# Kernel optimization log

Hardware: AMD Instinct MI355X
Metric: run time of the kernel (lower is better)

## Reference

```python
import jax, jax.numpy as jnp
import numpy as np
import math

B, H, S, D = 2, 16, 4096, 64

def setup_inputs() -> dict:
    key = jax.random.key(0)
    kq, kk, kv = jax.random.split(key, 3)
    q = jax.random.normal(kq, (B, H, S, D), dtype=jnp.float32)
    k = jax.random.normal(kk, (B, H, S, D), dtype=jnp.float32)
    v = jax.random.normal(kv, (B, H, S, D), dtype=jnp.float32)
    # causal mask: True above the diagonal means 'masked out' (matches masked_fill_)
    mask = ~jnp.tril(jnp.ones((S, S), dtype=bool))
    return {"q": q, "k": k, "v": v, "mask": mask}

def reference(q, k, v, mask):
    head_dim = q.shape[-1]
    scale = 1.0 / math.sqrt(head_dim)
    # scores: [B, H, S, S] -- same math as the chunked torch loop (chunking is a no-op mathematically)
    scores = jnp.einsum('bhqd,bhkd->bhqk', q, k) * scale
    scores = jnp.where(mask[None, None, :, :], -jnp.inf, scores)
    attn = jax.nn.softmax(scores, axis=-1)
    return jnp.einsum('bhqk,bhkd->bhqd', attn, v)
```

## Files before the change

kernel.cpp:

```cpp
#include <hip/hip_runtime.h>
#include <hip/hip_bf16.h>
#include <math.h>

#define SLEN 4096
#define DH   64
#define KVB  64
#define NHEAD 32
#define QBLK 128
#define NQT   (SLEN / QBLK)
#define TILE_E (KVB * DH)

typedef float  f32x4 __attribute__((ext_vector_type(4)));
typedef short  bf16x8 __attribute__((ext_vector_type(8)));
typedef unsigned short u16x8 __attribute__((ext_vector_type(8)));
typedef unsigned short u16x4 __attribute__((ext_vector_type(4)));
union U8 { u16x8 u; bf16x8 b; };
union U4 { unsigned d[4]; bf16x8 b; };

__device__ inline unsigned short f2bf(float f) {
    return __builtin_bit_cast(unsigned short, __float2bfloat16(f));
}
__device__ inline unsigned pk2(float lo, float hi_) {
    return (unsigned)f2bf(lo) | ((unsigned)f2bf(hi_) << 16);
}

__device__ inline void gload16(const unsigned short* g, unsigned short* l) {
    __builtin_amdgcn_global_load_lds(
        (const __attribute__((address_space(1))) void*)g,
        (__attribute__((address_space(3))) void*)l, 16, 0, 0);
}

extern "C" __global__ __launch_bounds__(512)
void prep_kv(const float* __restrict__ K, const float* __restrict__ V,
             unsigned short* __restrict__ Kb, unsigned short* __restrict__ Vt)
{
    const int tile = blockIdx.x & 63;
    const int head = blockIdx.x >> 6;
    const size_t gbase = (size_t)head * SLEN * DH + (size_t)tile * KVB * DH;
    const size_t tbase = ((size_t)head * 64 + tile) * TILE_E;
    const int tid = threadIdx.x;
    if (blockIdx.y == 0) {
        const int row = tid >> 3, d0 = (tid & 7) * 8;
        const float* src = K + gbase + (size_t)row * DH + d0;
        f32x4 a = *(const f32x4*)src, b = *(const f32x4*)(src + 4);
        u16x8 o;
        #pragma unroll
        for (int j = 0; j < 4; ++j) { o[j] = f2bf(a[j]); o[4 + j] = f2bf(b[j]); }
        *(u16x8*)&Kb[tbase + row * 64 + ((unsigned)d0 ^ ((row & 7) << 3))] = o;
    } else {
        const int kk = tid & 63, d0 = (tid >> 6) * 8;
        const int pos = ((kk >> 5) << 5) | (((kk & 15) >> 2) << 3)
                      | (((kk >> 4) & 1) << 2) | (kk & 3);
        const float* src = V + gbase + (size_t)kk * DH + d0;
        f32x4 a = *(const f32x4*)src, b = *(const f32x4*)(src + 4);
        #pragma unroll
        for (int j = 0; j < 8; ++j) {
            const int d = d0 + j;
            const float x = (j < 4) ? a[j] : b[j - 4];
            Vt[tbase + d * 64 + ((unsigned)pos ^ ((d & 7) << 3))] = f2bf(x);
        }
    }
}

extern "C" __global__ __launch_bounds__(256, 4)
void fa_fwd_v19(const float* __restrict__ Q, float* __restrict__ O,
                const unsigned short* __restrict__ Kb,
                const unsigned short* __restrict__ Vt)
{
    const int tid  = threadIdx.x;
    const int lane = tid & 63;
    const int w    = tid >> 6;
    const int l15  = lane & 15;
    const int l4   = lane >> 4;

    const int bid  = (int)blockIdx.x;
    const int i32  = bid >> 5;
    const int qt   = (i32 < 16) ? (2 * i32) : (63 - 2 * i32);
    const int head = bid & 31;
    const size_t qbase  = (size_t)head * SLEN * DH;
    const size_t kvbase = (size_t)head * 64 * TILE_E;

    __shared__ __align__(16) unsigned short Kl[3][TILE_E];
    __shared__ __align__(16) unsigned short Vl[2][TILE_E];

    const float QSC = 0.125f * 1.44269504088896340736f;

    U8 ones;
    #pragma unroll
    for (int j = 0; j < 8; ++j) ones.u[j] = 0x3F80;

    const unsigned short* ksrc = Kb + kvbase;
    const unsigned short* vsrc = Vt + kvbase;

    const int q0   = qt * QBLK;
    const int ntl  = 2 * qt + 2;
    const int wg0  = q0 + w * 16;
    const int wg1  = q0 + 64 + w * 16;
    const int qg0  = wg0 + l15;
    const int qg1  = wg1 + l15;

    auto stageK = [&](int b, int t) {
        const size_t toff = (size_t)t * TILE_E;
        const int ib = w * 2;
        gload16(ksrc + toff + ib * 512 + lane * 8,       &Kl[b][ib * 512]);
        gload16(ksrc + toff + (ib + 1) * 512 + lane * 8, &Kl[b][(ib + 1) * 512]);
    };
    auto stageV = [&](int b, int t) {
        const size_t toff = (size_t)t * TILE_E;
        const int ib = w * 2;
        gload16(vsrc + toff + ib * 512 + lane * 8,       &Vl[b][ib * 512]);
        gload16(vsrc + toff + (ib + 1) * 512 + lane * 8, &Vl[b][(ib + 1) * 512]);
    };

    stageK(0, 0);
    stageV(0, 0);
    stageK(1, 1);

    bf16x8 aq0[2], aq1[2];
    {
        const float* qp0 = Q + qbase + (size_t)qg0 * DH + l4 * 8;
        const float* qp1 = Q + qbase + (size_t)qg1 * DH + l4 * 8;
        #pragma unroll
        for (int ch = 0; ch < 2; ++ch) {
            f32x4 f0 = *(const f32x4*)(qp0 + ch * 32);
            f32x4 f1 = *(const f32x4*)(qp0 + ch * 32 + 4);
            U4 u;
            u.d[0] = pk2(f0[0] * QSC, f0[1] * QSC);
            u.d[1] = pk2(f0[2] * QSC, f0[3] * QSC);
            u.d[2] = pk2(f1[0] * QSC, f1[1] * QSC);
            u.d[3] = pk2(f1[2] * QSC, f1[3] * QSC);
            aq0[ch] = u.b;
            f0 = *(const f32x4*)(qp1 + ch * 32);
            f1 = *(const f32x4*)(qp1 + ch * 32 + 4);
            u.d[0] = pk2(f0[0] * QSC, f0[1] * QSC);
            u.d[1] = pk2(f0[2] * QSC, f0[3] * QSC);
            u.d[2] = pk2(f1[0] * QSC, f1[1] * QSC);
            u.d[3] = pk2(f1[2] * QSC, f1[3] * QSC);
            aq1[ch] = u.b;
        }
    }

    f32x4 acc0[4] = {}, acc1[4] = {};
    f32x4 lrow0 = {}, lrow1 = {};

    int kb = 0, vb = 0;
    for (int t = 0; t < ntl; ++t) {
        const int k0 = t * KVB;
        if (t + 1 < ntl) asm volatile("s_waitcnt vmcnt(2)" ::: "memory");
        else             asm volatile("s_waitcnt vmcnt(0)" ::: "memory");
        __builtin_amdgcn_s_barrier();

        if (t + 1 < ntl) stageV(vb ^ 1, t + 1);
        if (t + 2 < ntl) stageK((kb == 0) ? 2 : kb - 1, t + 2);

        {
            const bool live0 = (k0 <= wg0 + 15);
            const unsigned short* Kc = &Kl[kb][0];
            const unsigned short* Vc = &Vl[vb][0];

            __builtin_amdgcn_s_setprio(1);
            f32x4 s0[4], s1[4];
            #pragma unroll
            for (int nt = 0; nt < 4; ++nt) {
                const int row = nt * 16 + l15;
                const unsigned rb = (unsigned)row * 64, sw = (unsigned)((row & 7) << 3);
                U8 ak0, ak1;
                ak0.u = *(const u16x8*)&Kc[rb + ((unsigned)(l4 * 8) ^ sw)];
                ak1.u = *(const u16x8*)&Kc[rb + ((unsigned)(32 + l4 * 8) ^ sw)];
                if (live0) {
                    f32x4 z = {};
                    z = __builtin_amdgcn_mfma_f32_16x16x32_bf16(ak0.b, aq0[0], z, 0, 0, 0);
                    s0[nt] = __builtin_amdgcn_mfma_f32_16x16x32_bf16(ak1.b, aq0[1], z, 0, 0, 0);
                }
                f32x4 z1 = {};
                z1 = __builtin_amdgcn_mfma_f32_16x16x32_bf16(ak0.b, aq1[0], z1, 0, 0, 0);
                s1[nt] = __builtin_amdgcn_mfma_f32_16x16x32_bf16(ak1.b, aq1[1], z1, 0, 0, 0);
            }
            __builtin_amdgcn_s_setprio(0);

            if (live0 && (k0 + KVB - 1 > wg0)) {
                #pragma unroll
                for (int nt = 0; nt < 4; ++nt)
                    #pragma unroll
                    for (int r = 0; r < 4; ++r)
                        if (k0 + nt * 16 + l4 * 4 + r > qg0) s0[nt][r] = -INFINITY;
            }
            if (k0 + KVB - 1 > wg1) {
                #pragma unroll
                for (int nt = 0; nt < 4; ++nt)
                    #pragma unroll
                    for (int r = 0; r < 4; ++r)
                        if (k0 + nt * 16 + l4 * 4 + r > qg1) s1[nt][r] = -INFINITY;
            }

            U4 u00, u01, u10, u11;
            if (live0) {
                u00.d[0] = pk2(exp2f(s0[0][0]), exp2f(s0[0][1]));
                u00.d[1] = pk2(exp2f(s0[0][2]), exp2f(s0[0][3]));
                u00.d[2] = pk2(exp2f(s0[1][0]), exp2f(s0[1][1]));
                u00.d[3] = pk2(exp2f(s0[1][2]), exp2f(s0[1][3]));
                u01.d[0] = pk2(exp2f(s0[2][0]), exp2f(s0[2][1]));
                u01.d[1] = pk2(exp2f(s0[2][2]), exp2f(s0[2][3]));
                u01.d[2] = pk2(exp2f(s0[3][0]), exp2f(s0[3][1]));
                u01.d[3] = pk2(exp2f(s0[3][2]), exp2f(s0[3][3]));
            }
            u10.d[0] = pk2(exp2f(s1[0][0]), exp2f(s1[0][1]));
            u10.d[1] = pk2(exp2f(s1[0][2]), exp2f(s1[0][3]));
            u10.d[2] = pk2(exp2f(s1[1][0]), exp2f(s1[1][1]));
            u10.d[3] = pk2(exp2f(s1[1][2]), exp2f(s1[1][3]));
            u11.d[0] = pk2(exp2f(s1[2][0]), exp2f(s1[2][1]));
            u11.d[1] = pk2(exp2f(s1[2][2]), exp2f(s1[2][3]));
            u11.d[2] = pk2(exp2f(s1[3][0]), exp2f(s1[3][1]));
            u11.d[3] = pk2(exp2f(s1[3][2]), exp2f(s1[3][3]));

            __builtin_amdgcn_s_setprio(1);
            if (live0) {
                lrow0 = __builtin_amdgcn_mfma_f32_16x16x32_bf16(u00.b, ones.b, lrow0, 0, 0, 0);
                lrow0 = __builtin_amdgcn_mfma_f32_16x16x32_bf16(u01.b, ones.b, lrow0, 0, 0, 0);
            }
            lrow1 = __builtin_amdgcn_mfma_f32_16x16x32_bf16(u10.b, ones.b, lrow1, 0, 0, 0);
            lrow1 = __builtin_amdgcn_mfma_f32_16x16x32_bf16(u11.b, ones.b, lrow1, 0, 0, 0);
            #pragma unroll
            for (int nt = 0; nt < 4; ++nt) {
                const int row = nt * 16 + l15;
                const unsigned rb = (unsigned)row * 64, sw = (unsigned)((row & 7) << 3);
                U8 vb0, vb1;
                vb0.u = *(const u16x8*)&Vc[rb + ((unsigned)(l4 * 8) ^ sw)];
                vb1.u = *(const u16x8*)&Vc[rb + ((unsigned)(32 + l4 * 8) ^ sw)];
                if (live0) {
                    acc0[nt] = __builtin_amdgcn_mfma_f32_16x16x32_bf16(u00.b, vb0.b, acc0[nt], 0, 0, 0);
                    acc0[nt] = __builtin_amdgcn_mfma_f32_16x16x32_bf16(u01.b, vb1.b, acc0[nt], 0, 0, 0);
                }
                acc1[nt] = __builtin_amdgcn_mfma_f32_16x16x32_bf16(u10.b, vb0.b, acc1[nt], 0, 0, 0);
                acc1[nt] = __builtin_amdgcn_mfma_f32_16x16x32_bf16(u11.b, vb1.b, acc1[nt], 0, 0, 0);
            }
            __builtin_amdgcn_s_setprio(0);
        }

        kb = (kb == 2) ? 0 : kb + 1;
        vb ^= 1;
    }

    #pragma unroll
    for (int r = 0; r < 4; ++r) {
        const float inv0 = 1.f / lrow0[r];
        const float inv1 = 1.f / lrow1[r];
        float* op0 = O + qbase + (size_t)(wg0 + l4 * 4 + r) * DH + l15;
        float* op1 = O + qbase + (size_t)(wg1 + l4 * 4 + r) * DH + l15;
        #pragma unroll
        for (int nt = 0; nt < 4; ++nt) {
            op0[nt * 16] = acc0[nt][r] * inv0;
            op1[nt * 16] = acc1[nt][r] * inv1;
        }
    }
}

#define QBLK4 128
#define KPAD 72
#define NQT4  (SLEN/QBLK4)
#define NPAIR4 (NQT4/2)

extern "C" __global__ __launch_bounds__(256)
void fa_fwd_causal(const float* __restrict__ Q, const float* __restrict__ K,
                   const float* __restrict__ V, float* __restrict__ O)
{
    const int tid  = threadIdx.x;
    const int lane = tid & 63;
    const int w    = tid >> 6;
    const int l15  = lane & 15;
    const int l4   = lane >> 4;

    const int bid  = (int)blockIdx.x;
    const int work = (bid & 7) * (NPAIR4 * NHEAD / 8) + (bid >> 3);
    const int head = work >> 4;
    const int pr   = work & (NPAIR4 - 1);
    const size_t base = (size_t)head * SLEN * DH;

    __shared__ unsigned short Kl[2][KVB * KPAD];
    __shared__ unsigned short Vt[2][DH * KPAD];
    __shared__ unsigned short Plds[4][16 * KPAD];

    const float QSC = 0.125f * 1.44269504088896340736f;
    const int krow = tid >> 2,        kc0 = (tid & 3) * 16;
    const int vd0  = (tid >> 4) * 4,  vk0 = (tid & 15) * 4;

    #pragma unroll 1
    for (int ph = 0; ph < 2; ++ph) {
        const int qt  = ph ? (NQT4 - 1 - pr) : pr;
        const int q0  = qt * QBLK4;
        const int ntl = 2 * qt + 2;
        const int qwave = q0 + w * 32;

        bf16x8 aq[2][2];
        #pragma unroll
        for (int set = 0; set < 2; ++set) {
            const int qr = q0 + w * 32 + set * 16 + l15;
            const float* qp = Q + base + (size_t)qr * DH + l4 * 8;
            #pragma unroll
            for (int ch = 0; ch < 2; ++ch) {
                f32x4 f0 = *(const f32x4*)(qp + ch * 32);
                f32x4 f1 = *(const f32x4*)(qp + ch * 32 + 4);
                U8 u;
                #pragma unroll
                for (int j = 0; j < 4; ++j) { u.u[j] = f2bf(f0[j] * QSC); u.u[4 + j] = f2bf(f1[j] * QSC); }
                aq[set][ch] = u.b;
            }
        }

        f32x4 acc[2][4] = {};
        float mrun[2] = { -INFINITY, -INFINITY };
        float lrun[2] = { 0.f, 0.f };
        f32x4 kreg[4], vreg[4];

        auto g_load = [&](int t) {
            const float* kp = K + base + (size_t)(t * KVB + krow) * DH + kc0;
            #pragma unroll
            for (int i = 0; i < 4; ++i) kreg[i] = *(const f32x4*)(kp + i * 4);
            const float* vp = V + base + (size_t)(t * KVB + vk0) * DH + vd0;
            #pragma unroll
            for (int i = 0; i < 4; ++i) vreg[i] = *(const f32x4*)(vp + (size_t)i * DH);
        };
        auto s_write = [&](int c) {
            unsigned short tmp[16];
            #pragma unroll
            for (int i = 0; i < 4; ++i)
                #pragma unroll
                for (int j = 0; j < 4; ++j) tmp[i * 4 + j] = f2bf(kreg[i][j]);
            unsigned short* kd = &Kl[c][krow * KPAD + kc0];
            *(u16x8*)kd       = *(u16x8*)&tmp[0];
            *(u16x8*)(kd + 8) = *(u16x8*)&tmp[8];
            #pragma unroll
            for (int i = 0; i < 4; ++i) {
                u16x4 pk;
                pk[0] = f2bf(vreg[0][i]); pk[1] = f2bf(vreg[1][i]);
                pk[2] = f2bf(vreg[2][i]); pk[3] = f2bf(vreg[3][i]);
                *(u16x4*)&Vt[c][(vd0 + i) * KPAD + vk0] = pk;
            }
        };

        g_load(0); s_write(0); g_load(1);
        __syncthreads();

        for (int t = 0; t < ntl; ++t) {
            const int c  = t & 1;
            const int k0 = t * KVB;
            if (t + 1 < ntl) { s_write(c ^ 1); if (t + 2 < ntl) g_load(t + 2); }

            if (k0 <= qwave + 31) {
                #pragma unroll
                for (int set = 0; set < 2; ++set) {
                    const int qs0 = qwave + set * 16;
                    if (k0 > qs0 + 15) continue;
                    const int q = qs0 + l15;

                    f32x4 s[4];
                    #pragma unroll
                    for (int nt = 0; nt < 4; ++nt) {
                        U8 ak0, ak1;
                        ak0.u = *(const u16x8*)&Kl[c][(nt*16 + l15) * KPAD + l4*8];
                        ak1.u = *(const u16x8*)&Kl[c][(nt*16 + l15) * KPAD + 32 + l4*8];
                        f32x4 z = {};
                        z = __builtin_amdgcn_mfma_f32_16x16x32_bf16(ak0.b, aq[set][0], z, 0, 0, 0);
                        z = __builtin_amdgcn_mfma_f32_16x16x32_bf16(ak1.b, aq[set][1], z, 0, 0, 0);
                        s[nt] = z;
                    }
                    if (k0 + KVB - 1 > qs0) {
                        #pragma unroll
                        for (int nt = 0; nt < 4; ++nt)
                            #pragma unroll
                            for (int r = 0; r < 4; ++r)
                                if (k0 + nt*16 + l4*4 + r > q) s[nt][r] = -INFINITY;
                    }
                    float mx = s[0][0];
                    #pragma unroll
                    for (int nt = 0; nt < 4; ++nt)
                        #pragma unroll
                        for (int r = 0; r < 4; ++r)
                            if (!(nt == 0 && r == 0)) mx = fmaxf(mx, s[nt][r]);
                    mx = fmaxf(mx, __shfl_xor(mx, 16));
                    mx = fmaxf(mx, __shfl_xor(mx, 32));
                    float mn = fmaxf(mrun[set], mx);
                    float fr = exp2f(mrun[set] - mn);
                    mrun[set] = mn;
                    float p[4][4];
                    float rs = 0.f;
                    #pragma unroll
                    for (int nt = 0; nt < 4; ++nt)
                        #pragma unroll
                        for (int r = 0; r < 4; ++r) {
                            float e = exp2f(s[nt][r] - mn);
                            p[nt][r] = e; rs += e;
                        }
                    rs += __shfl_xor(rs, 16);
                    rs += __shfl_xor(rs, 32);
                    lrun[set] = lrun[set] * fr + rs;

                    unsigned short* Pw = &Plds[w][0];
                    #pragma unroll
                    for (int nt = 0; nt < 4; ++nt) {
                        u16x4 pk;
                        pk[0] = f2bf(p[nt][0]); pk[1] = f2bf(p[nt][1]);
                        pk[2] = f2bf(p[nt][2]); pk[3] = f2bf(p[nt][3]);
                        *(u16x4*)&Pw[l15 * KPAD + nt*16 + l4*4] = pk;
                    }
                    #pragma unroll
                    for (int r = 0; r < 4; ++r) {
                        float frr = __shfl(fr, l4*4 + r);
                        #pragma unroll
                        for (int nt = 0; nt < 4; ++nt) acc[set][nt][r] *= frr;
                    }
                    asm volatile("s_waitcnt lgkmcnt(0)" ::: "memory");
                    __builtin_amdgcn_sched_barrier(0);
                    U8 pa0, pa1;
                    pa0.u = *(const u16x8*)&Pw[l15 * KPAD + l4*8];
                    pa1.u = *(const u16x8*)&Pw[l15 * KPAD + 32 + l4*8];
                    #pragma unroll
                    for (int nt = 0; nt < 4; ++nt) {
                        U8 vb0, vb1;
                        vb0.u = *(const u16x8*)&Vt[c][(nt*16 + l15) * KPAD + l4*8];
                        vb1.u = *(const u16x8*)&Vt[c][(nt*16 + l15) * KPAD + 32 + l4*8];
                        acc[set][nt] = __builtin_amdgcn_mfma_f32_16x16x32_bf16(pa0.b, vb0.b, acc[set][nt], 0, 0, 0);
                        acc[set][nt] = __builtin_amdgcn_mfma_f32_16x16x32_bf16(pa1.b, vb1.b, acc[set][nt], 0, 0, 0);
                    }
                }
            }
            __syncthreads();
        }
        #pragma unroll
        for (int set = 0; set < 2; ++set) {
            float inv = 1.f / lrun[set];
            #pragma unroll
            for (int r = 0; r < 4; ++r) {
                float invr = __shfl(inv, l4*4 + r);
                const int qrow = q0 + w*32 + set*16 + l4*4 + r;
                float* op = O + base + (size_t)qrow * DH + l15;
                #pragma unroll
                for (int nt = 0; nt < 4; ++nt)
                    op[nt*16] = acc[set][nt][r] * invr;
            }
        }
        __syncthreads();
    }
}

extern "C" void kernel_launch(void* const* d_in, const int* in_sizes, int n_in,
                              void* d_out, int out_size, void* d_ws, size_t ws_size,
                              hipStream_t stream) {
    (void)in_sizes; (void)n_in; (void)out_size;
    const float* q = (const float*)d_in[0];
    const float* k = (const float*)d_in[1];
    const float* v = (const float*)d_in[2];
    float* o = (float*)d_out;

    const size_t kv_elems = (size_t)NHEAD * 64 * TILE_E;
    const size_t need = 2 * kv_elems * sizeof(unsigned short);
    if (ws_size >= need) {
        unsigned short* Kb = (unsigned short*)d_ws;
        unsigned short* Vtw = Kb + kv_elems;
        prep_kv<<<dim3(NHEAD * 64, 2), 512, 0, stream>>>(k, v, Kb, Vtw);
        fa_fwd_v19<<<dim3(NQT * NHEAD), 256, 0, stream>>>(q, o, Kb, Vtw);
    } else {
        fa_fwd_causal<<<dim3(NPAIR4 * NHEAD), 256, 0, stream>>>(q, k, v, o);
    }
}
```

Before: 151.1 us.

## Software-pipeline QK^T of tile t with PV of tile t-1 in causal FA

Restructures the main loop so each iteration issues the QK^T MFMAs for the current KV tile and then the PV and row-sum MFMAs for the previous tile's probabilities, which are kept in registers. The exp2 and packing work is moved after the MFMA block so it can overlap with matrix-core work. V gets a third LDS buffer, the wait counts are adjusted, and a drain step handles the last tile after the loop. The cost is extra registers and LDS, and the occupancy hint drops from 4 to 3 blocks per SIMD-group.

```diff
diff --git a/kernel.cpp b/kernel.cpp
--- a/kernel.cpp
+++ b/kernel.cpp
@@ -62,8 +62,8 @@
     }
 }
 
-extern "C" __global__ __launch_bounds__(256, 4)
-void fa_fwd_v19(const float* __restrict__ Q, float* __restrict__ O,
+extern "C" __global__ __launch_bounds__(256, 3)
+void fa_fwd_v21(const float* __restrict__ Q, float* __restrict__ O,
                 const unsigned short* __restrict__ Kb,
                 const unsigned short* __restrict__ Vt)
 {
@@ -81,7 +81,7 @@
     const size_t kvbase = (size_t)head * 64 * TILE_E;
 
     __shared__ __align__(16) unsigned short Kl[3][TILE_E];
-    __shared__ __align__(16) unsigned short Vl[2][TILE_E];
+    __shared__ __align__(16) unsigned short Vl[3][TILE_E];
 
     const float QSC = 0.125f * 1.44269504088896340736f;
 
@@ -142,84 +142,45 @@
 
     f32x4 acc0[4] = {}, acc1[4] = {};
     f32x4 lrow0 = {}, lrow1 = {};
-
-    int kb = 0, vb = 0;
+    U4 pu00, pu01, pu10, pu11;
+    bool prevL0 = false;
+
     for (int t = 0; t < ntl; ++t) {
         const int k0 = t * KVB;
-        if (t + 1 < ntl) asm volatile("s_waitcnt vmcnt(2)" ::: "memory");
-        else             asm volatile("s_waitcnt vmcnt(0)" ::: "memory");
+        if (t + 1 < ntl) asm volatile("s_waitcnt vmcnt(4)" ::: "memory");
+        else             asm volatile("s_waitcnt vmcnt(2)" ::: "memory");
         __builtin_amdgcn_s_barrier();
 
-        if (t + 1 < ntl) stageV(vb ^ 1, t + 1);
-        if (t + 2 < ntl) stageK((kb == 0) ? 2 : kb - 1, t + 2);
-
-        {
-            const bool live0 = (k0 <= wg0 + 15);
-            const unsigned short* Kc = &Kl[kb][0];
-            const unsigned short* Vc = &Vl[vb][0];
-
-            __builtin_amdgcn_s_setprio(1);
-            f32x4 s0[4], s1[4];
-            #pragma unroll
-            for (int nt = 0; nt < 4; ++nt) {
-                const int row = nt * 16 + l15;
-                const unsigned rb = (unsigned)row * 64, sw = (unsigned)((row & 7) << 3);
-                U8 ak0, ak1;
-                ak0.u = *(const u16x8*)&Kc[rb + ((unsigned)(l4 * 8) ^ sw)];
-                ak1.u = *(const u16x8*)&Kc[rb + ((unsigned)(32 + l4 * 8) ^ sw)];
-                if (live0) {
-                    f32x4 z = {};
-                    z = __builtin_amdgcn_mfma_f32_16x16x32_bf16(ak0.b, aq0[0], z, 0, 0, 0);
-                    s0[nt] = __builtin_amdgcn_mfma_f32_16x16x32_bf16(ak1.b, aq0[1], z, 0, 0, 0);
-                }
-                f32x4 z1 = {};
-                z1 = __builtin_amdgcn_mfma_f32_16x16x32_bf16(ak0.b, aq1[0], z1, 0, 0, 0);
-                s1[nt] = __builtin_amdgcn_mfma_f32_16x16x32_bf16(ak1.b, aq1[1], z1, 0, 0, 0);
-            }
-            __builtin_amdgcn_s_setprio(0);
-
-            if (live0 && (k0 + KVB - 1 > wg0)) {
-                #pragma unroll
-                for (int nt = 0; nt < 4; ++nt)
-                    #pragma unroll
-                    for (int r = 0; r < 4; ++r)
-                        if (k0 + nt * 16 + l4 * 4 + r > qg0) s0[nt][r] = -INFINITY;
-            }
-            if (k0 + KVB - 1 > wg1) {
-                #pragma unroll
-                for (int nt = 0; nt < 4; ++nt)
-                    #pragma unroll
-                    for (int r = 0; r < 4; ++r)
-                        if (k0 + nt * 16 + l4 * 4 + r > qg1) s1[nt][r] = -INFINITY;
-            }
-
-            U4 u00, u01, u10, u11;
+        const unsigned short* Kc = &Kl[t % 3][0];
+        const unsigned short* Vc = &Vl[(t + 2) % 3][0];
+        const bool live0 = (k0 <= wg0 + 15);
+
+        __builtin_amdgcn_s_setprio(1);
+        f32x4 s0[4], s1[4];
+        #pragma unroll
+        for (int nt = 0; nt < 4; ++nt) {
+            const int row = nt * 16 + l15;
+            const unsigned rb = (unsigned)row * 64, sw = (unsigned)((row & 7) << 3);
+            U8 ak0, ak1;
+            ak0.u = *(const u16x8*)&Kc[rb + ((unsigned)(l4 * 8) ^ sw)];
+            ak1.u = *(const u16x8*)&Kc[rb + ((unsigned)(32 + l4 * 8) ^ sw)];
             if (live0) {
-                u00.d[0] = pk2(exp2f(s0[0][0]), exp2f(s0[0][1]));
-                u00.d[1] = pk2(exp2f(s0[0][2]), exp2f(s0[0][3]));
-                u00.d[2] = pk2(exp2f(s0[1][0]), exp2f(s0[1][1]));
-                u00.d[3] = pk2(exp2f(s0[1][2]), exp2f(s0[1][3]));
-                u01.d[0] = pk2(exp2f(s0[2][0]), exp2f(s0[2][1]));
-                u01.d[1] = pk2(exp2f(s0[2][2]), exp2f(s0[2][3]));
-                u01.d[2] = pk2(exp2f(s0[3][0]), exp2f(s0[3][1]));
-                u01.d[3] = pk2(exp2f(s0[3][2]), exp2f(s0[3][3]));
-            }
-            u10.d[0] = pk2(exp2f(s1[0][0]), exp2f(s1[0][1]));
-            u10.d[1] = pk2(exp2f(s1[0][2]), exp2f(s1[0][3]));
-            u10.d[2] = pk2(exp2f(s1[1][0]), exp2f(s1[1][1]));
-            u10.d[3] = pk2(exp2f(s1[1][2]), exp2f(s1[1][3]));
-            u11.d[0] = pk2(exp2f(s1[2][0]), exp2f(s1[2][1]));
-            u11.d[1] = pk2(exp2f(s1[2][2]), exp2f(s1[2][3]));
-            u11.d[2] = pk2(exp2f(s1[3][0]), exp2f(s1[3][1]));
-            u11.d[3] = pk2(exp2f(s1[3][2]), exp2f(s1[3][3]));
-
-            __builtin_amdgcn_s_setprio(1);
-            if (live0) {
-                lrow0 = __builtin_amdgcn_mfma_f32_16x16x32_bf16(u00.b, ones.b, lrow0, 0, 0, 0);
-                lrow0 = __builtin_amdgcn_mfma_f32_16x16x32_bf16(u01.b, ones.b, lrow0, 0, 0, 0);
-            }
-            lrow1 = __builtin_amdgcn_mfma_f32_16x16x32_bf16(u10.b, ones.b, lrow1, 0, 0, 0);
-            lrow1 = __builtin_amdgcn_mfma_f32_16x16x32_bf16(u11.b, ones.b, lrow1, 0, 0, 0);
+                f32x4 z = {};
+                z = __builtin_amdgcn_mfma_f32_16x16x32_bf16(ak0.b, aq0[0], z, 0, 0, 0);
+                s0[nt] = __builtin_amdgcn_mfma_f32_16x16x32_bf16(ak1.b, aq0[1], z, 0, 0, 0);
+            }
+            f32x4 z1 = {};
+            z1 = __builtin_amdgcn_mfma_f32_16x16x32_bf16(ak0.b, aq1[0], z1, 0, 0, 0);
+            s1[nt] = __builtin_amdgcn_mfma_f32_16x16x32_bf16(ak1.b, aq1[1], z1, 0, 0, 0);
+        }
+
+        if (t > 0) {
+            if (prevL0) {
+                lrow0 = __builtin_amdgcn_mfma_f32_16x16x32_bf16(pu00.b, ones.b, lrow0, 0, 0, 0);
+                lrow0 = __builtin_amdgcn_mfma_f32_16x16x32_bf16(pu01.b, ones.b, lrow0, 0, 0, 0);
+            }
+            lrow1 = __builtin_amdgcn_mfma_f32_16x16x32_bf16(pu10.b, ones.b, lrow1, 0, 0, 0);
+            lrow1 = __builtin_amdgcn_mfma_f32_16x16x32_bf16(pu11.b, ones.b, lrow1, 0, 0, 0);
             #pragma unroll
             for (int nt = 0; nt < 4; ++nt) {
                 const int row = nt * 16 + l15;
@@ -227,18 +188,79 @@
                 U8 vb0, vb1;
                 vb0.u = *(const u16x8*)&Vc[rb + ((unsigned)(l4 * 8) ^ sw)];
                 vb1.u = *(const u16x8*)&Vc[rb + ((unsigned)(32 + l4 * 8) ^ sw)];
-                if (live0) {
-                    acc0[nt] = __builtin_amdgcn_mfma_f32_16x16x32_bf16(u00.b, vb0.b, acc0[nt], 0, 0, 0);
-                    acc0[nt] = __builtin_amdgcn_mfma_f32_16x16x32_bf16(u01.b, vb1.b, acc0[nt], 0, 0, 0);
+                if (prevL0) {
+                    acc0[nt] = __builtin_amdgcn_mfma_f32_16x16x32_bf16(pu00.b, vb0.b, acc0[nt], 0, 0, 0);
+                    acc0[nt] = __builtin_amdgcn_mfma_f32_16x16x32_bf16(pu01.b, vb1.b, acc0[nt], 0, 0, 0);
                 }
-                acc1[nt] = __builtin_amdgcn_mfma_f32_16x16x32_bf16(u10.b, vb0.b, acc1[nt], 0, 0, 0);
-                acc1[nt] = __builtin_amdgcn_mfma_f32_16x16x32_bf16(u11.b, vb1.b, acc1[nt], 0, 0, 0);
-            }
-            __builtin_amdgcn_s_setprio(0);
-        }
-
-        kb = (kb == 2) ? 0 : kb + 1;
-        vb ^= 1;
+                acc1[nt] = __builtin_amdgcn_mfma_f32_16x16x32_bf16(pu10.b, vb0.b, acc1[nt], 0, 0, 0);
+                acc1[nt] = __builtin_amdgcn_mfma_f32_16x16x32_bf16(pu11.b, vb1.b, acc1[nt], 0, 0, 0);
+            }
+        }
+        __builtin_amdgcn_s_setprio(0);
+
+        if (live0 && (k0 + KVB - 1 > wg0)) {
+            #pragma unroll
+            for (int nt = 0; nt < 4; ++nt)
+                #pragma unroll
+                for (int r = 0; r < 4; ++r)
+                    if (k0 + nt * 16 + l4 * 4 + r > qg0) s0[nt][r] = -INFINITY;
+        }
+        if (k0 + KVB - 1 > wg1) {
+            #pragma unroll
+            for (int nt = 0; nt < 4; ++nt)
+                #pragma unroll
+                for (int r = 0; r < 4; ++r)
+                    if (k0 + nt * 16 + l4 * 4 + r > qg1) s1[nt][r] = -INFINITY;
+        }
+
+        if (live0) {
+            pu00.d[0] = pk2(exp2f(s0[0][0]), exp2f(s0[0][1]));
+            pu00.d[1] = pk2(exp2f(s0[0][2]), exp2f(s0[0][3]));
+            pu00.d[2] = pk2(exp2f(s0[1][0]), exp2f(s0[1][1]));
+            pu00.d[3] = pk2(exp2f(s0[1][2]), exp2f(s0[1][3]));
+            pu01.d[0] = pk2(exp2f(s0[2][0]), exp2f(s0[2][1]));
+            pu01.d[1] = pk2(exp2f(s0[2][2]), exp2f(s0[2][3]));
+            pu01.d[2] = pk2(exp2f(s0[3][0]), exp2f(s0[3][1]));
+            pu01.d[3] = pk2(exp2f(s0[3][2]), exp2f(s0[3][3]));
+        }
+        pu10.d[0] = pk2(exp2f(s1[0][0]), exp2f(s1[0][1]));
+        pu10.d[1] = pk2(exp2f(s1[0][2]), exp2f(s1[0][3]));
+        pu10.d[2] = pk2(exp2f(s1[1][0]), exp2f(s1[1][1]));
+        pu10.d[3] = pk2(exp2f(s1[1][2]), exp2f(s1[1][3]));
+        pu11.d[0] = pk2(exp2f(s1[2][0]), exp2f(s1[2][1]));
+        pu11.d[1] = pk2(exp2f(s1[2][2]), exp2f(s1[2][3]));
+        pu11.d[2] = pk2(exp2f(s1[3][0]), exp2f(s1[3][1]));
+        pu11.d[3] = pk2(exp2f(s1[3][2]), exp2f(s1[3][3]));
+        prevL0 = live0;
+
+        if (t + 1 < ntl) stageV((t + 1) % 3, t + 1);
+        if (t + 2 < ntl) stageK((t + 2) % 3, t + 2);
+    }
+
+    asm volatile("s_waitcnt vmcnt(0)" ::: "memory");
+    __builtin_amdgcn_s_barrier();
+    {
+        const unsigned short* Vc = &Vl[(ntl + 2) % 3][0];
+        if (prevL0) {
+            lrow0 = __builtin_amdgcn_mfma_f32_16x16x32_bf16(pu00.b, ones.b, lrow0, 0, 0, 0);
+            lrow0 = __builtin_amdgcn_mfma_f32_16x16x32_bf16(pu01.b, ones.b, lrow0, 0, 0, 0);
+        }
+        lrow1 = __builtin_amdgcn_mfma_f32_16x16x32_bf16(pu10.b, ones.b, lrow1, 0, 0, 0);
+        lrow1 = __builtin_amdgcn_mfma_f32_16x16x32_bf16(pu11.b, ones.b, lrow1, 0, 0, 0);
+        #pragma unroll
+        for (int nt = 0; nt < 4; ++nt) {
+            const int row = nt * 16 + l15;
+            const unsigned rb = (unsigned)row * 64, sw = (unsigned)((row & 7) << 3);
+            U8 vb0, vb1;
+            vb0.u = *(const u16x8*)&Vc[rb + ((unsigned)(l4 * 8) ^ sw)];
+            vb1.u = *(const u16x8*)&Vc[rb + ((unsigned)(32 + l4 * 8) ^ sw)];
+            if (prevL0) {
+                acc0[nt] = __builtin_amdgcn_mfma_f32_16x16x32_bf16(pu00.b, vb0.b, acc0[nt], 0, 0, 0);
+                acc0[nt] = __builtin_amdgcn_mfma_f32_16x16x32_bf16(pu01.b, vb1.b, acc0[nt], 0, 0, 0);
+            }
+            acc1[nt] = __builtin_amdgcn_mfma_f32_16x16x32_bf16(pu10.b, vb0.b, acc1[nt], 0, 0, 0);
+            acc1[nt] = __builtin_amdgcn_mfma_f32_16x16x32_bf16(pu11.b, vb1.b, acc1[nt], 0, 0, 0);
+        }
     }
 
     #pragma unroll
@@ -458,7 +480,7 @@
         unsigned short* Kb = (unsigned short*)d_ws;
         unsigned short* Vtw = Kb + kv_elems;
         prep_kv<<<dim3(NHEAD * 64, 2), 512, 0, stream>>>(k, v, Kb, Vtw);
-        fa_fwd_v19<<<dim3(NQT * NHEAD), 256, 0, stream>>>(q, o, Kb, Vtw);
+        fa_fwd_v21<<<dim3(NQT * NHEAD), 256, 0, stream>>>(q, o, Kb, Vtw);
     } else {
         fa_fwd_causal<<<dim3(NPAIR4 * NHEAD), 256, 0, stream>>>(q, k, v, o);
     }
```

Result: faster. 126.8 us (-16.1%).
